# Optimization experiments

Measured on AMD Instinct MI355X. Metric: run time of the kernel, lower is better.

## Reference

```python
import jax, jax.numpy as jnp
import numpy as np

B, T, IN, H, OUT = 4096, 256, 2, 50, 2


def _rnn_layer(x, W_ih, W_hh, b_ih, b_hh):
    # x: [B, T, F] -> out: [B, T, H]. Elman RNN: h_t = tanh(W_ih x_t + b_ih + W_hh h_{t-1} + b_hh)
    pre = jnp.einsum('btf,hf->bth', x, W_ih) + b_ih + b_hh  # input projection hoisted out of scan
    h0 = jnp.zeros((x.shape[0], W_hh.shape[0]), dtype=x.dtype)

    def step(h, pre_t):
        h = jnp.tanh(pre_t + h @ W_hh.T)
        return h, h

    _, hs = jax.lax.scan(step, h0, jnp.swapaxes(pre, 0, 1))  # scan over time: [T, B, H]
    return jnp.swapaxes(hs, 0, 1)


def setup_inputs() -> dict:
    key = jax.random.key(0)
    ks = jax.random.split(key, 16)
    s_in = 1.0 / np.sqrt(H)  # torch nn.RNN init: U(-1/sqrt(H), 1/sqrt(H))

    def u(k, shape):
        return jax.random.uniform(k, shape, jnp.float32, -s_in, s_in)

    return {
        'x': jax.random.normal(ks[0], (B, T, IN), jnp.float32),
        'W_ih1': u(ks[1], (H, IN)), 'W_hh1': u(ks[2], (H, H)), 'b_ih1': u(ks[3], (H,)), 'b_hh1': u(ks[4], (H,)),
        'W_ih2': u(ks[5], (H, H)), 'W_hh2': u(ks[6], (H, H)), 'b_ih2': u(ks[7], (H,)), 'b_hh2': u(ks[8], (H,)),
        'W_ih3': u(ks[9], (H, H)), 'W_hh3': u(ks[10], (H, H)), 'b_ih3': u(ks[11], (H,)), 'b_hh3': u(ks[12], (H,)),
        'fc_w': u(ks[13], (OUT, H)), 'fc_b': u(ks[14], (OUT,)),
    }


def reference(x, W_ih1, W_hh1, b_ih1, b_hh1, W_ih2, W_hh2, b_ih2, b_hh2,
              W_ih3, W_hh3, b_ih3, b_hh3, fc_w, fc_b):
    out = _rnn_layer(x, W_ih1, W_hh1, b_ih1, b_hh1)
    out = _rnn_layer(out, W_ih2, W_hh2, b_ih2, b_hh2)
    out = _rnn_layer(out, W_ih3, W_hh3, b_ih3, b_hh3)
    return out[:, -1, :] @ fc_w.T + fc_b  # [B, OUT]
```

## Files before the change

### kernel.cpp

```cpp
#include <hip/hip_runtime.h>
#include <hip/hip_fp16.h>

namespace {

constexpr int T_STEPS = 256;
constexpr int HD = 50;
constexpr int HP = 64;
constexpr int KST = 88;
constexpr int KSTS = 72;
constexpr int BT = 16;
constexpr int NTHR = 768;
constexpr int XST = 34;
constexpr int LAY_SH = BT * KST;
constexpr int SLOT_SH = 3 * LAY_SH;

typedef __attribute__((ext_vector_type(8))) _Float16 f16x8;
typedef __attribute__((ext_vector_type(4))) float f32x4;

__device__ __forceinline__ unsigned short f2h(float x) {
  __half h = __float2half(x);
  return *reinterpret_cast<unsigned short*>(&h);
}
__device__ __forceinline__ float h2f(unsigned short u) {
  __half h;
  *reinterpret_cast<unsigned short*>(&h) = u;
  return __half2float(h);
}

#define MFMA16 __builtin_amdgcn_mfma_f32_16x16x32_f16

__global__ __launch_bounds__(NTHR, 3) void rnn3_kernel(
    const float* __restrict__ x,
    const float* __restrict__ Wih1, const float* __restrict__ Whh1,
    const float* __restrict__ bih1, const float* __restrict__ bhh1,
    const float* __restrict__ Wih2, const float* __restrict__ Whh2,
    const float* __restrict__ bih2, const float* __restrict__ bhh2,
    const float* __restrict__ Wih3, const float* __restrict__ Whh3,
    const float* __restrict__ bih3, const float* __restrict__ bhh3,
    const float* __restrict__ fcw, const float* __restrict__ fcb,
    float* __restrict__ out) {
  __shared__ unsigned short hbuf[3 * SLOT_SH];
  __shared__ float xls[T_STEPS][XST];
  __shared__ unsigned short scr[HP * KSTS];

  const int tid = threadIdx.x;
  const int w = tid >> 6;
  const int myL = w >> 2;
  const int wv = w & 3;
  const int lane = tid & 63;
  const int quad = lane >> 4;
  const int l15 = lane & 15;
  const int b0 = blockIdx.x * BT;

  {
    unsigned int* hz = reinterpret_cast<unsigned int*>(hbuf);
    const int n = 3 * SLOT_SH / 2;
    for (int i = tid; i < n; i += NTHR) hz[i] = 0u;
  }
  for (int idx = tid; idx < BT * T_STEPS; idx += NTHR) {
    int b = idx >> 8, t = idx & 255;
    float2 v = *reinterpret_cast<const float2*>(x + (size_t)(b0 + b) * (T_STEPS * 2) + 2 * t);
    xls[t][2 * b] = v.x;
    xls[t][2 * b + 1] = v.y;
  }

  const float* mats[5] = {Whh1, Wih2, Whh2, Wih3, Whh3};
  constexpr int matL[5] = {0, 1, 1, 2, 2};
  constexpr int matS[5] = {0, 0, 1, 0, 1};
  f16x8 wA[2][2];
#pragma unroll
  for (int sl = 0; sl < 2; ++sl)
#pragma unroll
    for (int ks = 0; ks < 2; ++ks) wA[sl][ks] = f16x8(0);

  const int arow = 16 * wv + l15;
#pragma unroll
  for (int m = 0; m < 5; ++m) {
    __syncthreads();
    const float* W = mats[m];
    for (int idx = tid; idx < HP * HP; idx += NTHR) {
      int i = idx >> 6, k = idx & 63;
      float v = (i < HD && k < HD) ? W[i * HD + k] : 0.0f;
      scr[i * KSTS + k] = f2h(v);
    }
    __syncthreads();
    if (myL == matL[m]) {
      const int sl = matS[m];
      const unsigned short* ph = &scr[arow * KSTS + 8 * quad];
      wA[sl][0] = *reinterpret_cast<const f16x8*>(ph);
      wA[sl][1] = *reinterpret_cast<const f16x8*>(ph + 32);
    }
  }

  const int ic = 16 * wv + 4 * quad;
  const float* bi = (myL == 0) ? bih1 : (myL == 1) ? bih2 : bih3;
  const float* bh = (myL == 0) ? bhh1 : (myL == 1) ? bhh2 : bhh3;
  float wx0[4], wx1[4];
  f32x4 bsv;
#pragma unroll
  for (int r = 0; r < 4; ++r) {
    int i = ic + r;
    bool v = i < HD;
    bsv[r] = v ? (bi[i] + bh[i]) : 0.0f;
    wx0[r] = (v && myL == 0) ? Wih1[i * 2 + 0] : 0.0f;
    wx1[r] = (v && myL == 0) ? Wih1[i * 2 + 1] : 0.0f;
  }

  const int selfBuf = myL;
  const int crossBuf = (myL > 0) ? myL - 1 : 0;
  const int ldsOff = l15 * KST + 8 * quad;

  const unsigned short* sbase = hbuf + selfBuf * LAY_SH + ldsOff;
  const unsigned short* cbase = hbuf + crossBuf * LAY_SH + ldsOff;
  unsigned short* wbase = hbuf + myL * LAY_SH + l15 * KST + ic;

  f16x8 pfC0 = f16x8(0), pfC1 = f16x8(0);

  __syncthreads();

  auto step = [&](int s, int wr, int rd, bool act) {
    f16x8 bS0, bS1, pfN0, pfN1;
    if (act) {
      bS0 = *reinterpret_cast<const f16x8*>(sbase + rd * SLOT_SH);
      bS1 = *reinterpret_cast<const f16x8*>(sbase + rd * SLOT_SH + 32);
    }
    if (myL > 0) {
      pfN0 = *reinterpret_cast<const f16x8*>(cbase + rd * SLOT_SH);
      pfN1 = *reinterpret_cast<const f16x8*>(cbase + rd * SLOT_SH + 32);
    }
    if (act) {
      f32x4 c;
      if (myL == 0) {
        float2 xc = *reinterpret_cast<const float2*>(&xls[s][2 * l15]);
        f32x4 ci;
#pragma unroll
        for (int r = 0; r < 4; ++r) ci[r] = fmaf(wx1[r], xc.y, fmaf(wx0[r], xc.x, bsv[r]));
        c = MFMA16(wA[0][0], bS0, ci, 0, 0, 0);
        c = MFMA16(wA[0][1], bS1, c, 0, 0, 0);
      } else {
        c = MFMA16(wA[0][0], pfC0, bsv, 0, 0, 0);
        c = MFMA16(wA[0][1], pfC1, c, 0, 0, 0);
        c = MFMA16(wA[1][0], bS0, c, 0, 0, 0);
        c = MFMA16(wA[1][1], bS1, c, 0, 0, 0);
      }
      float d[4];
#pragma unroll
      for (int r = 0; r < 4; ++r) {
        float xr = __builtin_amdgcn_fmed3f(c[r], -11.0f, 11.0f);
        d[r] = __expf(2.0f * xr) + 1.0f;
      }
      float p01 = d[0] * d[1], p23 = d[2] * d[3];
      float rp = __builtin_amdgcn_rcpf(p01 * p23);
      float q01 = rp * p23, q23 = rp * p01;
      float iv[4] = {q01 * d[1], q01 * d[0], q23 * d[3], q23 * d[2]};
      unsigned short ht[4];
#pragma unroll
      for (int r = 0; r < 4; ++r) ht[r] = f2h(fmaf(-2.0f, iv[r], 1.0f));
      unsigned int h01 = (unsigned int)ht[0] | ((unsigned int)ht[1] << 16);
      unsigned int h23 = (unsigned int)ht[2] | ((unsigned int)ht[3] << 16);
      *reinterpret_cast<uint2*>(wbase + wr * SLOT_SH) = make_uint2(h01, h23);
    }
    if (myL > 0) { pfC0 = pfN0; pfC1 = pfN1; }
    __syncthreads();
  };

  auto actOf = [&](int s) {
    return (myL == 0) ? (s < T_STEPS)
         : (myL == 1) ? (s >= 2 && s < T_STEPS + 2)
                      : (s >= 4);
  };

  for (int s = 0; s < 4; ++s) step(s, s % 3, (s + 2) % 3, actOf(s));
  for (int sb = 4; sb < 256; sb += 3) {
    step(sb + 0, 1, 0, true);
    step(sb + 1, 2, 1, true);
    step(sb + 2, 0, 2, true);
  }
  for (int s = 256; s < 260; ++s) step(s, s % 3, (s + 2) % 3, actOf(s));

  if (tid < BT * 2) {
    int b = tid >> 1, o = tid & 1;
    const unsigned short* h3 = hbuf + 1 * SLOT_SH + 2 * LAY_SH + b * KST;
    float acc = fcb[o];
    for (int i = 0; i < HD; ++i) acc += fcw[o * HD + i] * h2f(h3[i]);
    out[(size_t)(b0 + b) * 2 + o] = acc;
  }
}

}

extern "C" void kernel_launch(void* const* d_in, const int* in_sizes, int n_in,
                              void* d_out, int out_size, void* d_ws, size_t ws_size,
                              hipStream_t stream) {
  const float* x = (const float*)d_in[0];
  const float* Wih1 = (const float*)d_in[1];
  const float* Whh1 = (const float*)d_in[2];
  const float* bih1 = (const float*)d_in[3];
  const float* bhh1 = (const float*)d_in[4];
  const float* Wih2 = (const float*)d_in[5];
  const float* Whh2 = (const float*)d_in[6];
  const float* bih2 = (const float*)d_in[7];
  const float* bhh2 = (const float*)d_in[8];
  const float* Wih3 = (const float*)d_in[9];
  const float* Whh3 = (const float*)d_in[10];
  const float* bih3 = (const float*)d_in[11];
  const float* bhh3 = (const float*)d_in[12];
  const float* fcw = (const float*)d_in[13];
  const float* fcb = (const float*)d_in[14];

  rnn3_kernel<<<4096 / BT, NTHR, 0, stream>>>(x, Wih1, Whh1, bih1, bhh1,
                                              Wih2, Whh2, bih2, bhh2,
                                              Wih3, Whh3, bih3, bhh3,
                                              fcw, fcb, (float*)d_out);
}
```

Before: 196.9 us.

## Replace per-step block barriers with LDS atomic counters between layer wavefronts

In the steady-state part of the time loop, the per-step __syncthreads is replaced by workgroup-scope atomic counters in LDS, one per layer. Each wave spins until its own layer, the previous layer and the next layer have advanced far enough, so that 4-wave layer groups no longer wait on the whole block. This aims to remove full-block barrier stalls and let layers drift relative to one another. It adds busy-wait polling and atomics, and relies on the triple-buffer slot reuse staying correct under the looser ordering.

Result: slower. 218.1 us (+10.8%).

```diff
diff --git a/kernel.cpp b/kernel.cpp
--- a/kernel.cpp
+++ b/kernel.cpp
@@ -42,6 +42,7 @@
   __shared__ unsigned short hbuf[3 * SLOT_SH];
   __shared__ float xls[T_STEPS][XST];
   __shared__ unsigned short scr[HP * KSTS];
+  __shared__ int wc[3];
 
   const int tid = threadIdx.x;
   const int w = tid >> 6;
@@ -56,6 +57,7 @@
     unsigned int* hz = reinterpret_cast<unsigned int*>(hbuf);
     const int n = 3 * SLOT_SH / 2;
     for (int i = tid; i < n; i += NTHR) hz[i] = 0u;
+    if (tid < 3) wc[tid] = 0;
   }
   for (int idx = tid; idx < BT * T_STEPS; idx += NTHR) {
     int b = idx >> 8, t = idx & 255;
@@ -118,50 +120,45 @@
 
   __syncthreads();
 
-  auto step = [&](int s, int wr, int rd, bool act) {
-    f16x8 bS0, bS1, pfN0, pfN1;
-    if (act) {
-      bS0 = *reinterpret_cast<const f16x8*>(sbase + rd * SLOT_SH);
-      bS1 = *reinterpret_cast<const f16x8*>(sbase + rd * SLOT_SH + 32);
-    }
+  auto core = [&](int s, int wr, int rd) {
+    f16x8 bS0 = *reinterpret_cast<const f16x8*>(sbase + rd * SLOT_SH);
+    f16x8 bS1 = *reinterpret_cast<const f16x8*>(sbase + rd * SLOT_SH + 32);
+    f16x8 pfN0, pfN1;
     if (myL > 0) {
       pfN0 = *reinterpret_cast<const f16x8*>(cbase + rd * SLOT_SH);
       pfN1 = *reinterpret_cast<const f16x8*>(cbase + rd * SLOT_SH + 32);
     }
-    if (act) {
-      f32x4 c;
-      if (myL == 0) {
-        float2 xc = *reinterpret_cast<const float2*>(&xls[s][2 * l15]);
-        f32x4 ci;
-#pragma unroll
-        for (int r = 0; r < 4; ++r) ci[r] = fmaf(wx1[r], xc.y, fmaf(wx0[r], xc.x, bsv[r]));
-        c = MFMA16(wA[0][0], bS0, ci, 0, 0, 0);
-        c = MFMA16(wA[0][1], bS1, c, 0, 0, 0);
-      } else {
-        c = MFMA16(wA[0][0], pfC0, bsv, 0, 0, 0);
-        c = MFMA16(wA[0][1], pfC1, c, 0, 0, 0);
-        c = MFMA16(wA[1][0], bS0, c, 0, 0, 0);
-        c = MFMA16(wA[1][1], bS1, c, 0, 0, 0);
-      }
-      float d[4];
-#pragma unroll
-      for (int r = 0; r < 4; ++r) {
-        float xr = __builtin_amdgcn_fmed3f(c[r], -11.0f, 11.0f);
-        d[r] = __expf(2.0f * xr) + 1.0f;
-      }
-      float p01 = d[0] * d[1], p23 = d[2] * d[3];
-      float rp = __builtin_amdgcn_rcpf(p01 * p23);
-      float q01 = rp * p23, q23 = rp * p01;
-      float iv[4] = {q01 * d[1], q01 * d[0], q23 * d[3], q23 * d[2]};
-      unsigned short ht[4];
-#pragma unroll
-      for (int r = 0; r < 4; ++r) ht[r] = f2h(fmaf(-2.0f, iv[r], 1.0f));
-      unsigned int h01 = (unsigned int)ht[0] | ((unsigned int)ht[1] << 16);
-      unsigned int h23 = (unsigned int)ht[2] | ((unsigned int)ht[3] << 16);
-      *reinterpret_cast<uint2*>(wbase + wr * SLOT_SH) = make_uint2(h01, h23);
-    }
+    f32x4 c;
+    if (myL == 0) {
+      float2 xc = *reinterpret_cast<const float2*>(&xls[s][2 * l15]);
+      f32x4 ci;
+#pragma unroll
+      for (int r = 0; r < 4; ++r) ci[r] = fmaf(wx1[r], xc.y, fmaf(wx0[r], xc.x, bsv[r]));
+      c = MFMA16(wA[0][0], bS0, ci, 0, 0, 0);
+      c = MFMA16(wA[0][1], bS1, c, 0, 0, 0);
+    } else {
+      c = MFMA16(wA[0][0], pfC0, bsv, 0, 0, 0);
+      c = MFMA16(wA[0][1], pfC1, c, 0, 0, 0);
+      c = MFMA16(wA[1][0], bS0, c, 0, 0, 0);
+      c = MFMA16(wA[1][1], bS1, c, 0, 0, 0);
+    }
+    float d[4];
+#pragma unroll
+    for (int r = 0; r < 4; ++r) {
+      float xr = __builtin_amdgcn_fmed3f(c[r], -11.0f, 11.0f);
+      d[r] = __expf(2.0f * xr) + 1.0f;
+    }
+    float p01 = d[0] * d[1], p23 = d[2] * d[3];
+    float rp = __builtin_amdgcn_rcpf(p01 * p23);
+    float q01 = rp * p23, q23 = rp * p01;
+    float iv[4] = {q01 * d[1], q01 * d[0], q23 * d[3], q23 * d[2]};
+    unsigned short ht[4];
+#pragma unroll
+    for (int r = 0; r < 4; ++r) ht[r] = f2h(fmaf(-2.0f, iv[r], 1.0f));
+    unsigned int h01 = (unsigned int)ht[0] | ((unsigned int)ht[1] << 16);
+    unsigned int h23 = (unsigned int)ht[2] | ((unsigned int)ht[3] << 16);
+    *reinterpret_cast<uint2*>(wbase + wr * SLOT_SH) = make_uint2(h01, h23);
     if (myL > 0) { pfC0 = pfN0; pfC1 = pfN1; }
-    __syncthreads();
   };
 
   auto actOf = [&](int s) {
@@ -170,13 +167,43 @@
                       : (s >= 4);
   };
 
-  for (int s = 0; s < 4; ++s) step(s, s % 3, (s + 2) % 3, actOf(s));
-  for (int sb = 4; sb < 256; sb += 3) {
-    step(sb + 0, 1, 0, true);
-    step(sb + 1, 2, 1, true);
-    step(sb + 2, 0, 2, true);
-  }
-  for (int s = 256; s < 260; ++s) step(s, s % 3, (s + 2) % 3, actOf(s));
+  auto stepB = [&](int s, int wr, int rd, bool act) {
+    if (act) core(s, wr, rd);
+    else if (myL > 0) {
+      pfC0 = *reinterpret_cast<const f16x8*>(cbase + rd * SLOT_SH);
+      pfC1 = *reinterpret_cast<const f16x8*>(cbase + rd * SLOT_SH + 32);
+    }
+    __syncthreads();
+  };
+
+  int hvS = 0, hvC = 0, hvW = 0;
+  auto spin = [&](int idx, int t, int hv) {
+    if (hv >= t) return;
+    while (__hip_atomic_load(&wc[idx], __ATOMIC_ACQUIRE, __HIP_MEMORY_SCOPE_WORKGROUP) < t) {}
+  };
+  auto stepF = [&](int s, int wr, int rd, int tgt) {
+    spin(myL, tgt, hvS);
+    if (myL > 0) spin(myL - 1, tgt, hvC);
+    if (myL < 2) spin(myL + 1, tgt - 4, hvW);
+    core(s, wr, rd);
+    if (lane == 0)
+      __hip_atomic_fetch_add(&wc[myL], 1, __ATOMIC_RELEASE, __HIP_MEMORY_SCOPE_WORKGROUP);
+    hvS = __hip_atomic_load(&wc[myL], __ATOMIC_ACQUIRE, __HIP_MEMORY_SCOPE_WORKGROUP);
+    if (myL > 0) hvC = __hip_atomic_load(&wc[myL - 1], __ATOMIC_ACQUIRE, __HIP_MEMORY_SCOPE_WORKGROUP);
+    if (myL < 2) hvW = __hip_atomic_load(&wc[myL + 1], __ATOMIC_ACQUIRE, __HIP_MEMORY_SCOPE_WORKGROUP);
+  };
+
+  for (int s = 0; s < 8; ++s) stepB(s, s % 3, (s + 2) % 3, actOf(s));
+  int tgt = 0;
+  for (int g = 0; g < 80; ++g) {
+    int s = 8 + 3 * g;
+    stepF(s,     2, 1, tgt);
+    stepF(s + 1, 0, 2, tgt + 4);
+    stepF(s + 2, 1, 0, tgt + 8);
+    tgt += 12;
+  }
+  __syncthreads();
+  for (int s = 248; s < 260; ++s) stepB(s, s % 3, (s + 2) % 3, actOf(s));
 
   if (tid < BT * 2) {
     int b = tid >> 1, o = tid & 1;
```
